# Optimization experiments

Hardware: AMD Instinct MI355X
Metric: run time of the kernel (lower is better)

The kernel has to match this reference:

```python
import jax, jax.numpy as jnp
import numpy as np

IDIM1, IDIM2, HDIM = 512, 512, 256
EPS = 1e-5

def _layernorm(x, g, b):
    mu = jnp.mean(x, axis=-1, keepdims=True)
    var = jnp.var(x, axis=-1, keepdims=True)
    return (x - mu) * jax.lax.rsqrt(var + EPS) * g + b

def setup_inputs() -> dict:
    key = jax.random.key(0)
    ks = jax.random.split(key, 8)
    B, N, T = 16, 32, 256
    s1 = 1.0 / np.sqrt(IDIM1)
    s2 = 1.0 / np.sqrt(IDIM2)
    s3 = 1.0 / np.sqrt(HDIM)
    return {
        "x1": jax.random.normal(ks[0], (B, N, IDIM1), jnp.float32),
        "x2": jax.random.normal(ks[1], (B, T, IDIM2), jnp.float32),
        "W1": jax.random.uniform(ks[2], (IDIM1, HDIM), jnp.float32, -s1, s1),
        "b1": jax.random.uniform(ks[3], (HDIM,), jnp.float32, -s1, s1),
        "W2": jax.random.uniform(ks[4], (IDIM2, HDIM), jnp.float32, -s2, s2),
        "b2": jax.random.uniform(ks[5], (HDIM,), jnp.float32, -s2, s2),
        "W3": jax.random.uniform(ks[6], (HDIM, HDIM), jnp.float32, -s3, s3),
        "b3": jax.random.uniform(ks[7], (HDIM,), jnp.float32, -s3, s3),
        "g_norm": jnp.ones((HDIM,), jnp.float32),
        "be_norm": jnp.zeros((HDIM,), jnp.float32),
        "g_norm1": jnp.ones((HDIM,), jnp.float32),
        "be_norm1": jnp.zeros((HDIM,), jnp.float32),
    }

def reference(x1, x2, W1, b1, W2, b2, W3, b3, g_norm, be_norm, g_norm1, be_norm1):
    h1 = jax.nn.relu(x1 @ W1 + b1)          # [B,N,H]
    h2 = jax.nn.relu(x2 @ W2 + b2)          # [B,T,H]
    x = h1[:, :, None, :] * h2[:, None, :, :]  # [B,N,T,H] broadcast Hadamard
    x = _layernorm(x, g_norm, be_norm)
    x = x @ W3 + b3
    return jax.nn.relu(_layernorm(x, g_norm1, be_norm1))
```

## Files before the change

kernel.cpp:

```cpp
#include <hip/hip_runtime.h>
#include <hip/hip_bf16.h>
#include <stdint.h>

#define BB 16
#define NN 32
#define TT 256
#define HH 256
#define DD 512
#define EPSF 1e-5f

#define TROWS 32
#define ASTRIDE 264

typedef __attribute__((ext_vector_type(8))) short short8;
typedef __attribute__((ext_vector_type(4))) float floatx4;

__device__ __forceinline__ unsigned short f2bf(float f) {
    union { float f; unsigned u; } v; v.f = f;
    unsigned u = v.u;
    unsigned r = u + 0x7FFFu + ((u >> 16) & 1u);
    return (unsigned short)(r >> 16);
}
__device__ __forceinline__ float bf2f(unsigned short h) {
    union { unsigned u; float f; } v; v.u = ((unsigned)h) << 16;
    return v.f;
}

__global__ __launch_bounds__(256) void prep_kernel(
    const float* __restrict__ x1, const float* __restrict__ x2,
    const float* __restrict__ W1, const float* __restrict__ b1,
    const float* __restrict__ W2, const float* __restrict__ b2,
    const float* __restrict__ W3,
    float* __restrict__ h1, float* __restrict__ h2,
    unsigned short* __restrict__ W3p_hi, unsigned short* __restrict__ W3p_lo)
{
    const int blk = blockIdx.x;
    const int tid = threadIdx.x;

    if (blk >= 1152) {
        const int p  = (blk - 1152) * 256 + tid;
        const int o0 = p * 16;
        unsigned short thi[16], tlo[16];
#pragma unroll
        for (int e = 0; e < 16; ++e) {
            const int o    = o0 + e;
            const int j    = o & 7;
            const int lane = (o >> 3) & 63;
            const int kk   = (o >> 9) & 7;
            const int ct   = o >> 12;
            const int krow = kk * 32 + (lane >> 4) * 8 + j;
            const int col  = ct * 16 + (lane & 15);
            const float w  = W3[krow * HH + col];
            const unsigned short hi = f2bf(w);
            thi[e] = hi;
            tlo[e] = f2bf(w - bf2f(hi));
        }
        unsigned wh[8], wl[8];
#pragma unroll
        for (int e = 0; e < 8; ++e) {
            wh[e] = (unsigned)thi[2 * e] | ((unsigned)thi[2 * e + 1] << 16);
            wl[e] = (unsigned)tlo[2 * e] | ((unsigned)tlo[2 * e + 1] << 16);
        }
        uint4* dh = reinterpret_cast<uint4*>(W3p_hi + o0);
        dh[0] = make_uint4(wh[0], wh[1], wh[2], wh[3]);
        dh[1] = make_uint4(wh[4], wh[5], wh[6], wh[7]);
        uint4* dl = reinterpret_cast<uint4*>(W3p_lo + o0);
        dl[0] = make_uint4(wl[0], wl[1], wl[2], wl[3]);
        dl[1] = make_uint4(wl[4], wl[5], wl[6], wl[7]);
        return;
    }

    __shared__ float xs[8][DD];

    const int rowgrp  = blk >> 1;
    const int colbase = (blk & 1) * 128;

    const float* x; const float* W; const float* bias; float* h; int row0;
    if (rowgrp < 64) { x = x1; W = W1; bias = b1; h = h1; row0 = rowgrp * 8; }
    else             { x = x2; W = W2; bias = b2; h = h2; row0 = (rowgrp - 64) * 8; }

    {
        const float4* xg = reinterpret_cast<const float4*>(x + (size_t)row0 * DD);
        float4* xl = reinterpret_cast<float4*>(&xs[0][0]);
#pragma unroll
        for (int i = 0; i < 4; ++i) xl[tid + 256 * i] = xg[tid + 256 * i];
    }
    __syncthreads();

    const int jj  = tid & 127;
    const int rh  = tid >> 7;
    const int col = colbase + jj;

    float acc[4] = {0.0f, 0.0f, 0.0f, 0.0f};
    const float* Wp = W + col;

    for (int k = 0; k < DD; k += 8) {
        float w[8];
#pragma unroll
        for (int q = 0; q < 8; ++q) w[q] = Wp[(size_t)(k + q) * HH];
#pragma unroll
        for (int r = 0; r < 4; ++r) {
            const float4 xa = *reinterpret_cast<const float4*>(&xs[rh * 4 + r][k]);
            const float4 xb = *reinterpret_cast<const float4*>(&xs[rh * 4 + r][k + 4]);
            float s = acc[r];
            s = fmaf(xa.x, w[0], s); s = fmaf(xa.y, w[1], s);
            s = fmaf(xa.z, w[2], s); s = fmaf(xa.w, w[3], s);
            s = fmaf(xb.x, w[4], s); s = fmaf(xb.y, w[5], s);
            s = fmaf(xb.z, w[6], s); s = fmaf(xb.w, w[7], s);
            acc[r] = s;
        }
    }

    const float bb = bias[col];
#pragma unroll
    for (int r = 0; r < 4; ++r) {
        const float v = acc[r] + bb;
        h[(size_t)(row0 + rh * 4 + r) * HH + col] = v > 0.0f ? v : 0.0f;
    }
}

__global__ __launch_bounds__(256) void fused_mfma_kernel(
    const float* __restrict__ h1, const float* __restrict__ h2,
    const unsigned short* __restrict__ W3p_hi,
    const unsigned short* __restrict__ W3p_lo,
    const float* __restrict__ b3,
    const float* __restrict__ g0, const float* __restrict__ be0,
    const float* __restrict__ g1, const float* __restrict__ be1,
    float* __restrict__ out)
{
    __shared__ __align__(16) unsigned short Ah_s[TROWS * ASTRIDE];
    __shared__ __align__(16) unsigned short Al_s[TROWS * ASTRIDE];
    __shared__ float2 Spart[TROWS][4];
    __shared__ float2 LNP[TROWS];

    const int tid  = threadIdx.x;
    const int wave = tid >> 6;
    const int lane = tid & 63;
    const int blk  = blockIdx.x;
    const int tile = blk & 7;
    const int n    = (blk >> 3) & 31;
    const int b    = blk >> 8;

    {
        const float* h1row = h1 + ((size_t)b * NN + n) * HH;
        const float4 h1v  = *reinterpret_cast<const float4*>(h1row + 4 * lane);
        const float4 g0v  = *reinterpret_cast<const float4*>(g0  + 4 * lane);
        const float4 be0v = *reinterpret_cast<const float4*>(be0 + 4 * lane);
        const float* h2b  = h2 + ((size_t)b * TT + tile * TROWS) * HH;

#pragma unroll 2
        for (int i = 0; i < 8; ++i) {
            const int r = wave * 8 + i;
            float4 v = *reinterpret_cast<const float4*>(h2b + (size_t)r * HH + 4 * lane);
            v.x *= h1v.x; v.y *= h1v.y; v.z *= h1v.z; v.w *= h1v.w;
            float s = v.x + v.y + v.z + v.w;
            float q = v.x * v.x + v.y * v.y + v.z * v.z + v.w * v.w;
#pragma unroll
            for (int off = 32; off >= 1; off >>= 1) {
                s += __shfl_xor(s, off, 64);
                q += __shfl_xor(q, off, 64);
            }
            const float mu  = s * (1.0f / HH);
            const float var = q * (1.0f / HH) - mu * mu;
            const float rs  = rsqrtf(var + EPSF);
            float af[4];
            af[0] = (v.x - mu) * rs * g0v.x + be0v.x;
            af[1] = (v.y - mu) * rs * g0v.y + be0v.y;
            af[2] = (v.z - mu) * rs * g0v.z + be0v.z;
            af[3] = (v.w - mu) * rs * g0v.w + be0v.w;
            ushort4 ahi, alo;
            ahi.x = f2bf(af[0]); alo.x = f2bf(af[0] - bf2f(ahi.x));
            ahi.y = f2bf(af[1]); alo.y = f2bf(af[1] - bf2f(ahi.y));
            ahi.z = f2bf(af[2]); alo.z = f2bf(af[2] - bf2f(ahi.z));
            ahi.w = f2bf(af[3]); alo.w = f2bf(af[3] - bf2f(ahi.w));
            *reinterpret_cast<ushort4*>(&Ah_s[r * ASTRIDE + 4 * lane]) = ahi;
            *reinterpret_cast<ushort4*>(&Al_s[r * ASTRIDE + 4 * lane]) = alo;
        }
    }
    __syncthreads();

    const int m  = lane & 15;
    const int qd = lane >> 4;

    floatx4 acc[2][4];
#pragma unroll
    for (int ct = 0; ct < 4; ++ct) {
        const float bv = b3[wave * 64 + ct * 16 + m];
#pragma unroll
        for (int rt = 0; rt < 2; ++rt) {
            acc[rt][ct][0] = bv; acc[rt][ct][1] = bv;
            acc[rt][ct][2] = bv; acc[rt][ct][3] = bv;
        }
    }

#pragma unroll 2
    for (int kk = 0; kk < 8; ++kk) {
        short8 bh[4], bl[4];
#pragma unroll
        for (int ct = 0; ct < 4; ++ct) {
            const size_t off = ((size_t)((wave * 4 + ct) * 8 + kk) * 64 + lane) * 8;
            bh[ct] = *reinterpret_cast<const short8*>(W3p_hi + off);
            bl[ct] = *reinterpret_cast<const short8*>(W3p_lo + off);
        }
#pragma unroll
        for (int rt = 0; rt < 2; ++rt) {
            const int aoff = (rt * 16 + m) * ASTRIDE + kk * 32 + qd * 8;
            const short8 ah = *reinterpret_cast<const short8*>(&Ah_s[aoff]);
            const short8 al = *reinterpret_cast<const short8*>(&Al_s[aoff]);
#pragma unroll
            for (int ct = 0; ct < 4; ++ct) {
                floatx4 c = acc[rt][ct];
                c = __builtin_amdgcn_mfma_f32_16x16x32_bf16(ah, bh[ct], c, 0, 0, 0);
                c = __builtin_amdgcn_mfma_f32_16x16x32_bf16(al, bh[ct], c, 0, 0, 0);
                c = __builtin_amdgcn_mfma_f32_16x16x32_bf16(ah, bl[ct], c, 0, 0, 0);
                acc[rt][ct] = c;
            }
        }
    }

    {
        float ssum[8], qsum[8];
#pragma unroll
        for (int rt = 0; rt < 2; ++rt)
#pragma unroll
            for (int reg = 0; reg < 4; ++reg) {
                float s = 0.0f, q = 0.0f;
#pragma unroll
                for (int ct = 0; ct < 4; ++ct) {
                    const float y = acc[rt][ct][reg];
                    s += y; q = fmaf(y, y, q);
                }
                ssum[rt * 4 + reg] = s; qsum[rt * 4 + reg] = q;
            }
#pragma unroll
        for (int off = 1; off < 16; off <<= 1) {
#pragma unroll
            for (int e = 0; e < 8; ++e) {
                ssum[e] += __shfl_xor(ssum[e], off, 64);
                qsum[e] += __shfl_xor(qsum[e], off, 64);
            }
        }
        if (m == 0) {
#pragma unroll
            for (int rt = 0; rt < 2; ++rt)
#pragma unroll
                for (int reg = 0; reg < 4; ++reg) {
                    const int row = rt * 16 + qd * 4 + reg;
                    Spart[row][wave] = make_float2(ssum[rt * 4 + reg], qsum[rt * 4 + reg]);
                }
        }
    }
    __syncthreads();

    if (tid < TROWS) {
        float s = 0.0f, q = 0.0f;
#pragma unroll
        for (int w = 0; w < 4; ++w) {
            const float2 p = Spart[tid][w];
            s += p.x; q += p.y;
        }
        const float mu  = s * (1.0f / HH);
        const float var = q * (1.0f / HH) - mu * mu;
        LNP[tid] = make_float2(mu, rsqrtf(var + EPSF));
    }
    __syncthreads();

    {
        const int colb = wave * 64;
        float g1c[4], be1c[4];
#pragma unroll
        for (int ct = 0; ct < 4; ++ct) {
            g1c[ct]  = g1[colb + ct * 16 + m];
            be1c[ct] = be1[colb + ct * 16 + m];
        }
        float* outb = out + (((size_t)b * NN + n) * TT + tile * TROWS) * HH;

#pragma unroll
        for (int rt = 0; rt < 2; ++rt)
#pragma unroll
            for (int reg = 0; reg < 4; ++reg) {
                const int row = rt * 16 + qd * 4 + reg;
                const float2 p = LNP[row];
#pragma unroll
                for (int ct = 0; ct < 4; ++ct) {
                    const float y = acc[rt][ct][reg];
                    const float o = fmaxf((y - p.x) * p.y * g1c[ct] + be1c[ct], 0.0f);
                    outb[(size_t)row * HH + colb + ct * 16 + m] = o;
                }
            }
    }
}

extern "C" void kernel_launch(void* const* d_in, const int* in_sizes, int n_in,
                              void* d_out, int out_size, void* d_ws, size_t ws_size,
                              hipStream_t stream) {
    const float* x1  = (const float*)d_in[0];
    const float* x2  = (const float*)d_in[1];
    const float* W1  = (const float*)d_in[2];
    const float* b1  = (const float*)d_in[3];
    const float* W2  = (const float*)d_in[4];
    const float* b2  = (const float*)d_in[5];
    const float* W3  = (const float*)d_in[6];
    const float* b3  = (const float*)d_in[7];
    const float* g0  = (const float*)d_in[8];
    const float* be0 = (const float*)d_in[9];
    const float* g1  = (const float*)d_in[10];
    const float* be1 = (const float*)d_in[11];
    float* out = (float*)d_out;

    float* h1 = (float*)d_ws;
    float* h2 = h1 + (size_t)BB * NN * HH;
    unsigned short* W3p_hi = (unsigned short*)(h2 + (size_t)BB * TT * HH);
    unsigned short* W3p_lo = W3p_hi + (size_t)HH * HH;

    hipLaunchKernelGGL(prep_kernel, dim3(1168), dim3(256), 0, stream,
                       x1, x2, W1, b1, W2, b2, W3, h1, h2, W3p_hi, W3p_lo);

    hipLaunchKernelGGL(fused_mfma_kernel, dim3(4096), dim3(256), 0, stream,
                       h1, h2, W3p_hi, W3p_lo, b3, g0, be0, g1, be1, out);
}
```

Before: 254.8 us.

## Swizzle LDS A-tiles, truncation-based bf16 split, reuse LDS, raise occupancy

Replaces the padded LDS layout (stride 264) with an unpadded 512-byte row layout that uses an XOR swizzle to avoid bank conflicts, cutting shared memory per block. It aliases the LN-stat scratch arrays onto the A tiles behind an extra barrier and adds a launch-bounds occupancy hint of 5 blocks. It replaces round-to-nearest bf16 hi/lo splitting with a truncation-based split packed two values per word. It also batches the prologue row reductions four at a time for more ILP. The truncated hi part slightly changes the split error, and the occupancy hint may force register spilling.

```diff
diff --git a/kernel.cpp b/kernel.cpp
--- a/kernel.cpp
+++ b/kernel.cpp
@@ -10,7 +10,7 @@
 #define EPSF 1e-5f
 
 #define TROWS 32
-#define ASTRIDE 264
+#define ROWB  512
 
 typedef __attribute__((ext_vector_type(8))) short short8;
 typedef __attribute__((ext_vector_type(4))) float floatx4;
@@ -24,6 +24,19 @@
 __device__ __forceinline__ float bf2f(unsigned short h) {
     union { unsigned u; float f; } v; v.u = ((unsigned)h) << 16;
     return v.f;
+}
+
+__device__ __forceinline__ void split2(float f0, float f1, unsigned& hp, unsigned& lp) {
+    union { float f; unsigned u; } a0, a1, r0, r1;
+    a0.f = f0; a1.f = f1;
+    const unsigned h0 = a0.u & 0xFFFF0000u;
+    const unsigned h1 = a1.u & 0xFFFF0000u;
+    union { unsigned u; float f; } b0, b1;
+    b0.u = h0; b1.u = h1;
+    r0.f = f0 - b0.f;
+    r1.f = f1 - b1.f;
+    hp = (a0.u >> 16) | h1;
+    lp = (r0.u >> 16) | (r1.u & 0xFFFF0000u);
 }
 
 __global__ __launch_bounds__(256) void prep_kernel(
@@ -119,7 +132,7 @@
     }
 }
 
-__global__ __launch_bounds__(256) void fused_mfma_kernel(
+__global__ __launch_bounds__(256, 5) void fused_mfma_kernel(
     const float* __restrict__ h1, const float* __restrict__ h2,
     const unsigned short* __restrict__ W3p_hi,
     const unsigned short* __restrict__ W3p_lo,
@@ -128,10 +141,8 @@
     const float* __restrict__ g1, const float* __restrict__ be1,
     float* __restrict__ out)
 {
-    __shared__ __align__(16) unsigned short Ah_s[TROWS * ASTRIDE];
-    __shared__ __align__(16) unsigned short Al_s[TROWS * ASTRIDE];
-    __shared__ float2 Spart[TROWS][4];
-    __shared__ float2 LNP[TROWS];
+    __shared__ __align__(16) unsigned short Ah_s[TROWS * 256];
+    __shared__ __align__(16) unsigned short Al_s[TROWS * 256];
 
     const int tid  = threadIdx.x;
     const int wave = tid >> 6;
@@ -148,33 +159,47 @@
         const float4 be0v = *reinterpret_cast<const float4*>(be0 + 4 * lane);
         const float* h2b  = h2 + ((size_t)b * TT + tile * TROWS) * HH;
 
-#pragma unroll 2
-        for (int i = 0; i < 8; ++i) {
-            const int r = wave * 8 + i;
-            float4 v = *reinterpret_cast<const float4*>(h2b + (size_t)r * HH + 4 * lane);
-            v.x *= h1v.x; v.y *= h1v.y; v.z *= h1v.z; v.w *= h1v.w;
-            float s = v.x + v.y + v.z + v.w;
-            float q = v.x * v.x + v.y * v.y + v.z * v.z + v.w * v.w;
+#pragma unroll
+        for (int half = 0; half < 2; ++half) {
+            float4 v[4]; float s[4], q[4];
+#pragma unroll
+            for (int i = 0; i < 4; ++i) {
+                const int r = wave * 8 + half * 4 + i;
+                v[i] = *reinterpret_cast<const float4*>(h2b + (size_t)r * HH + 4 * lane);
+                v[i].x *= h1v.x; v[i].y *= h1v.y; v[i].z *= h1v.z; v[i].w *= h1v.w;
+                s[i] = v[i].x + v[i].y + v[i].z + v[i].w;
+                q[i] = v[i].x * v[i].x + v[i].y * v[i].y
+                     + v[i].z * v[i].z + v[i].w * v[i].w;
+            }
 #pragma unroll
             for (int off = 32; off >= 1; off >>= 1) {
-                s += __shfl_xor(s, off, 64);
-                q += __shfl_xor(q, off, 64);
-            }
-            const float mu  = s * (1.0f / HH);
-            const float var = q * (1.0f / HH) - mu * mu;
-            const float rs  = rsqrtf(var + EPSF);
-            float af[4];
-            af[0] = (v.x - mu) * rs * g0v.x + be0v.x;
-            af[1] = (v.y - mu) * rs * g0v.y + be0v.y;
-            af[2] = (v.z - mu) * rs * g0v.z + be0v.z;
-            af[3] = (v.w - mu) * rs * g0v.w + be0v.w;
-            ushort4 ahi, alo;
-            ahi.x = f2bf(af[0]); alo.x = f2bf(af[0] - bf2f(ahi.x));
-            ahi.y = f2bf(af[1]); alo.y = f2bf(af[1] - bf2f(ahi.y));
-            ahi.z = f2bf(af[2]); alo.z = f2bf(af[2] - bf2f(ahi.z));
-            ahi.w = f2bf(af[3]); alo.w = f2bf(af[3] - bf2f(ahi.w));
-            *reinterpret_cast<ushort4*>(&Ah_s[r * ASTRIDE + 4 * lane]) = ahi;
-            *reinterpret_cast<ushort4*>(&Al_s[r * ASTRIDE + 4 * lane]) = alo;
+#pragma unroll
+                for (int i = 0; i < 4; ++i) {
+                    s[i] += __shfl_xor(s[i], off, 64);
+                    q[i] += __shfl_xor(q[i], off, 64);
+                }
+            }
+#pragma unroll
+            for (int i = 0; i < 4; ++i) {
+                const int r = wave * 8 + half * 4 + i;
+                const float mu  = s[i] * (1.0f / HH);
+                const float var = q[i] * (1.0f / HH) - mu * mu;
+                const float rs  = rsqrtf(var + EPSF);
+                float af0 = (v[i].x - mu) * rs * g0v.x + be0v.x;
+                float af1 = (v[i].y - mu) * rs * g0v.y + be0v.y;
+                float af2 = (v[i].z - mu) * rs * g0v.z + be0v.z;
+                float af3 = (v[i].w - mu) * rs * g0v.w + be0v.w;
+                unsigned hp0, lp0, hp1, lp1;
+                split2(af0, af1, hp0, lp0);
+                split2(af2, af3, hp1, lp1);
+                const int byteoff = (lane * 8) ^ ((r & 7) << 4);
+                *reinterpret_cast<uint2*>(
+                    reinterpret_cast<char*>(Ah_s) + r * ROWB + byteoff)
+                    = make_uint2(hp0, hp1);
+                *reinterpret_cast<uint2*>(
+                    reinterpret_cast<char*>(Al_s) + r * ROWB + byteoff)
+                    = make_uint2(lp0, lp1);
+            }
         }
     }
     __syncthreads();
@@ -192,6 +217,9 @@
             acc[rt][ct][2] = bv; acc[rt][ct][3] = bv;
         }
     }
+
+    const char* AhB = reinterpret_cast<const char*>(Ah_s);
+    const char* AlB = reinterpret_cast<const char*>(Al_s);
 
 #pragma unroll 2
     for (int kk = 0; kk < 8; ++kk) {
@@ -202,11 +230,12 @@
             bh[ct] = *reinterpret_cast<const short8*>(W3p_hi + off);
             bl[ct] = *reinterpret_cast<const short8*>(W3p_lo + off);
         }
+        const int swzoff = (kk * 64 + qd * 16) ^ ((m & 7) << 4);
 #pragma unroll
         for (int rt = 0; rt < 2; ++rt) {
-            const int aoff = (rt * 16 + m) * ASTRIDE + kk * 32 + qd * 8;
-            const short8 ah = *reinterpret_cast<const short8*>(&Ah_s[aoff]);
-            const short8 al = *reinterpret_cast<const short8*>(&Al_s[aoff]);
+            const int rowbyte = (rt * 16 + m) * ROWB;
+            const short8 ah = *reinterpret_cast<const short8*>(AhB + rowbyte + swzoff);
+            const short8 al = *reinterpret_cast<const short8*>(AlB + rowbyte + swzoff);
 #pragma unroll
             for (int ct = 0; ct < 4; ++ct) {
                 floatx4 c = acc[rt][ct];
@@ -218,8 +247,8 @@
         }
     }
 
+    float ssum[8], qsum[8];
     {
-        float ssum[8], qsum[8];
 #pragma unroll
         for (int rt = 0; rt < 2; ++rt)
 #pragma unroll
@@ -240,15 +269,20 @@
                 qsum[e] += __shfl_xor(qsum[e], off, 64);
             }
         }
-        if (m == 0) {
-#pragma unroll
-            for (int rt = 0; rt < 2; ++rt)
-#pragma unroll
-                for (int reg = 0; reg < 4; ++reg) {
-                    const int row = rt * 16 + qd * 4 + reg;
-                    Spart[row][wave] = make_float2(ssum[rt * 4 + reg], qsum[rt * 4 + reg]);
-                }
-        }
+    }
+
+    __syncthreads();
+    float2* Spart = reinterpret_cast<float2*>(Ah_s);
+    float2* LNP   = reinterpret_cast<float2*>(Al_s);
+
+    if (m == 0) {
+#pragma unroll
+        for (int rt = 0; rt < 2; ++rt)
+#pragma unroll
+            for (int reg = 0; reg < 4; ++reg) {
+                const int row = rt * 16 + qd * 4 + reg;
+                Spart[row * 4 + wave] = make_float2(ssum[rt * 4 + reg], qsum[rt * 4 + reg]);
+            }
     }
     __syncthreads();
 
@@ -256,7 +290,7 @@
         float s = 0.0f, q = 0.0f;
 #pragma unroll
         for (int w = 0; w < 4; ++w) {
-            const float2 p = Spart[tid][w];
+            const float2 p = Spart[tid * 4 + w];
             s += p.x; q += p.y;
         }
         const float mu  = s * (1.0f / HH);
```

Result: slower. 262.3 us (+2.9%).
